# Kernel optimization log

Hardware: AMD Instinct MI355X
Metric: run time of the kernel (lower is better)

## Reference

```python
import jax, jax.numpy as jnp
import numpy as np
import math

S, H, NH, HD = 2048, 1280, 16, 80
WIN = 64
NW = S // WIN
I = 3420
OUT = 3584
L = 8
FULL_IDX = (3, 7)
MERGE = 4  # spatial_merge_size**2
EPS = 1e-6


def setup_inputs() -> dict:
    key = jax.random.key(0)
    ks = jax.random.split(key, 16)
    w = lambda k, s: jax.random.normal(k, s, jnp.float32) * 0.02
    # rotary tables: half-dim freqs duplicated, as in Qwen2.5-VL vision rotary
    inv_freq = 1.0 / (10000.0 ** (np.arange(0, HD // 2, dtype=np.float32) / (HD // 2)))
    freqs = np.outer(np.arange(S, dtype=np.float32), inv_freq)  # [S, HD/2]
    emb = np.concatenate([freqs, freqs], axis=-1)               # [S, HD]
    return {
        "hidden_states": jax.random.normal(ks[0], (S, H), jnp.float32),
        "full_attn_masks": jnp.ones((1, 1, S, S), jnp.float32),
        "window_attn_masks": jnp.ones((NW, 1, WIN, WIN), jnp.float32),
        "cos": jnp.asarray(np.cos(emb)),
        "sin": jnp.asarray(np.sin(emb)),
        "qkv_w": w(ks[1], (L, 3 * H, H)),
        "qkv_b": w(ks[2], (L, 3 * H)),
        "proj_w": w(ks[3], (L, H, H)),
        "proj_b": w(ks[4], (L, H)),
        "norm1_w": jnp.ones((L, H), jnp.float32),
        "norm2_w": jnp.ones((L, H), jnp.float32),
        "gate_w": w(ks[5], (L, I, H)),
        "gate_b": w(ks[6], (L, I)),
        "up_w": w(ks[7], (L, I, H)),
        "up_b": w(ks[8], (L, I)),
        "down_w": w(ks[9], (L, H, I)),
        "down_b": w(ks[10], (L, H)),
        "ln_q_w": jnp.ones((H,), jnp.float32),
        "m0_w": w(ks[11], (H * MERGE, H * MERGE)),
        "m0_b": w(ks[12], (H * MERGE,)),
        "m2_w": w(ks[13], (OUT, H * MERGE)),
        "m2_b": w(ks[14], (OUT,)),
    }


def rmsnorm(x, w):
    v = jnp.mean(jnp.square(x.astype(jnp.float32)), axis=-1, keepdims=True)
    return (x * jax.lax.rsqrt(v + EPS)) * w


def rotate_half(x):
    x1, x2 = jnp.split(x, 2, axis=-1)
    return jnp.concatenate([-x2, x1], axis=-1)


def apply_rope(q, k, cos, sin):
    return q * cos + rotate_half(q) * sin, k * cos + rotate_half(k) * sin


def attn_full(x, mask, cos, sin, qkv_w, qkv_b, proj_w, proj_b):
    # x: [S, H]; mask: [1, 1, S, S] (additive)
    qkv = (x @ qkv_w.T + qkv_b).reshape(S, 3, NH, HD)
    q, k, v = [t[:, i].transpose(1, 0, 2) for i, t in [(0, qkv), (1, qkv), (2, qkv)]]  # [NH, S, HD]
    q, k = apply_rope(q, k, cos, sin)  # cos/sin [S, HD] broadcast over heads
    aw = jnp.einsum('hsd,htd->hst', q, k) / math.sqrt(HD) + mask[0]
    aw = jax.nn.softmax(aw.astype(jnp.float32), axis=-1)
    o = jnp.einsum('hst,htd->hsd', aw, v).transpose(1, 0, 2).reshape(S, NH * HD)
    return o @ proj_w.T + proj_b


def attn_window(x, mask, cos, sin, qkv_w, qkv_b, proj_w, proj_b):
    xw = x.reshape(NW, WIN, H)
    qkv = (xw @ qkv_w.T + qkv_b).reshape(NW, WIN, 3, NH, HD).transpose(2, 0, 3, 1, 4)
    q, k, v = qkv[0], qkv[1], qkv[2]
    cw = cos.reshape(NW, 1, WIN, HD)
    sw = sin.reshape(NW, 1, WIN, HD)
    q, k = apply_rope(q, k, cw, sw)
    aw = jnp.einsum('whsd,whtd->whst', q, k) / math.sqrt(HD) + mask
    aw = jax.nn.softmax(aw.astype(jnp.float32), axis=-1)
    o = jnp.einsum('whst,whtd->whsd', aw, v).transpose(0, 2, 1, 3).reshape(S, NH * HD)
    return o @ proj_w.T + proj_b


def reference(hidden_states, full_attn_masks, window_attn_masks, cos, sin,
              qkv_w, qkv_b, proj_w, proj_b, norm1_w, norm2_w,
              gate_w, gate_b, up_w, up_b, down_w, down_b,
              ln_q_w, m0_w, m0_b, m2_w, m2_b):
    NEG = jnp.finfo(jnp.float32).min
    fm = (1.0 - full_attn_masks) * NEG
    wm = (1.0 - window_attn_masks) * NEG
    x = hidden_states
    for i in range(L):
        h = rmsnorm(x, norm1_w[i])
        if i in FULL_IDX:
            a = attn_full(h, fm, cos, sin, qkv_w[i], qkv_b[i], proj_w[i], proj_b[i])
        else:
            a = attn_window(h, wm, cos, sin, qkv_w[i], qkv_b[i], proj_w[i], proj_b[i])
        x = x + a
        h = rmsnorm(x, norm2_w[i])
        mlp = (jax.nn.silu(h @ gate_w[i].T + gate_b[i]) * (h @ up_w[i].T + up_b[i])) @ down_w[i].T + down_b[i]
        x = x + mlp
    # patch merger: RMSNorm -> merge 4 tokens -> Linear-GELU-Linear
    h = rmsnorm(x, ln_q_w).reshape(-1, H * MERGE)  # [S/4, 5120]
    h = jax.nn.gelu(h @ m0_w.T + m0_b, approximate=False)
    return h @ m2_w.T + m2_b  # [S/4, OUT]
```

## Files before the change

kernel.cpp:

```cpp
#include <hip/hip_runtime.h>
#include <hip/hip_bf16.h>
#include <math.h>

#define S_LEN 2048
#define HID   1280
#define NHEADS 16
#define HDIM  80
#define HDP   96
#define VROWS 96
#define LAYERS 8
#define IDIM  3420
#define IDIMP 3456
#define MERGED 5120
#define OUTD  3584
#define NCH   8
#define CHLEN 256
#define LWE   19824640LL

typedef __attribute__((ext_vector_type(8))) short short8;
typedef __attribute__((ext_vector_type(4))) float f32x4;
typedef __attribute__((ext_vector_type(16))) float f32x16;
typedef unsigned int u32;
typedef __attribute__((ext_vector_type(4))) u32 u32x4;
typedef __attribute__((address_space(1))) const u32* gptr_t;
typedef __attribute__((address_space(3))) u32* lptr_t;

__device__ inline unsigned short f2b(float f){
  __hip_bfloat16 b = __float2bfloat16(f);
  return __builtin_bit_cast(unsigned short, b);
}
__device__ inline float b2f(unsigned short u){
  return __bfloat162float(__builtin_bit_cast(__hip_bfloat16, u));
}
__device__ inline unsigned pk2(float lo, float hi){
  return (unsigned)f2b(lo) | ((unsigned)f2b(hi) << 16);
}

#define NSEG 42
struct ConvSegs {
  int bpre[NSEG + 1];
  long long srcoff[NSEG];
  long long dstoff[NSEG];
  int srcbase[NSEG];
  int N[NSEG], K[NSEG], Kp[NSEG];
  int rstride[NSEG], roffs[NSEG];
};

__global__ __launch_bounds__(256) void convert_all_kernel(
    ConvSegs cs,
    const float* __restrict__ b0, const float* __restrict__ b1,
    const float* __restrict__ b2, const float* __restrict__ b3,
    const float* __restrict__ b4, const float* __restrict__ b5,
    const float* __restrict__ b6,
    unsigned short* __restrict__ dst)
{
  const int b = blockIdx.x;
  int seg = 0;
  while (seg < NSEG - 1 && cs.bpre[seg + 1] <= b) ++seg;
  const int Kp = cs.Kp[seg], K = cs.K[seg], N = cs.N[seg];
  const int kg = Kp >> 3;
  size_t g = (size_t)(b - cs.bpre[seg]) * 256 + threadIdx.x;
  int k8 = (int)(g % kg);
  int n  = (int)(g / kg);
  int k0 = k8 * 8;
  const float* base;
  switch (cs.srcbase[seg]){
    case 0: base = b0; break; case 1: base = b1; break;
    case 2: base = b2; break; case 3: base = b3; break;
    case 4: base = b4; break; case 5: base = b5; break;
    default: base = b6; break;
  }
  const float* src = base + cs.srcoff[seg];
  u32 out0, out1, out2, out3;
  if (n < N && k0 + 8 <= K){
    const float* s = src + (size_t)n * K + k0;
    f32x4 f0 = __builtin_nontemporal_load((const f32x4*)s);
    f32x4 f1 = __builtin_nontemporal_load((const f32x4*)(s + 4));
    out0 = pk2(f0[0], f0[1]); out1 = pk2(f0[2], f0[3]);
    out2 = pk2(f1[0], f1[1]); out3 = pk2(f1[2], f1[3]);
  } else {
    u32 tmp[4];
    #pragma unroll
    for (int j = 0; j < 4; ++j){
      int ka = k0 + 2 * j;
      float lv = (n < N && ka     < K) ? src[(size_t)n * K + ka]     : 0.f;
      float hv = (n < N && ka + 1 < K) ? src[(size_t)n * K + ka + 1] : 0.f;
      tmp[j] = pk2(lv, hv);
    }
    out0 = tmp[0]; out1 = tmp[1]; out2 = tmp[2]; out3 = tmp[3];
  }
  size_t de = (size_t)cs.dstoff[seg] +
              ((size_t)n * cs.rstride[seg] + cs.roffs[seg]) * Kp + k0;
  u32x4 ov = {out0, out1, out2, out3};
  __builtin_nontemporal_store(ov, (u32x4*)(dst + de));
}

__global__ __launch_bounds__(256) void concat_bias_kernel(
    const float* __restrict__ g, const float* __restrict__ u, float* __restrict__ o)
{
  int L = blockIdx.y;
  int n = blockIdx.x * 256 + threadIdx.x;
  if (n >= 2 * IDIMP) return;
  int c = n >> 1, which = n & 1;
  float v = 0.f;
  if (c < IDIM) v = which ? u[(size_t)L * IDIM + c] : g[(size_t)L * IDIM + c];
  o[(size_t)L * 2 * IDIMP + n] = v;
}

__global__ __launch_bounds__(256) void rmsnorm_kernel(
    const float* __restrict__ x, const float* __restrict__ w,
    unsigned short* __restrict__ out, int H)
{
  int s = blockIdx.x;
  const float* row = x + (size_t)s * H;
  float ss = 0.f;
  for (int c = threadIdx.x; c < H; c += 256){ float v = row[c]; ss += v * v; }
  #pragma unroll
  for (int off = 32; off >= 1; off >>= 1) ss += __shfl_xor(ss, off, 64);
  __shared__ float red[4];
  if ((threadIdx.x & 63) == 0) red[threadIdx.x >> 6] = ss;
  __syncthreads();
  ss = red[0] + red[1] + red[2] + red[3];
  float rs = rsqrtf(ss / H + 1e-6f);
  unsigned short* orow = out + (size_t)s * H;
  for (int c = threadIdx.x; c < H; c += 256) orow[c] = f2b(row[c] * rs * w[c]);
}

template<int EPI, int BM>
__global__ __launch_bounds__(256) void gemm_kernel(
    const unsigned short* __restrict__ A, int lda,
    const unsigned short* __restrict__ B, int ldb,
    const float* __restrict__ bias, int Nact,
    void* __restrict__ Cv, int ldc,
    const float* __restrict__ res,
    int K)
{
  constexpr int MI = BM / 32;
  __shared__ __align__(16) unsigned short As[2][BM * 32];
  __shared__ __align__(16) unsigned short Bs[2][4096];
  const int tid  = threadIdx.x;
  const int lane = tid & 63;
  const int wave = tid >> 6;
  const int wm = wave >> 1, wn = wave & 1;
  const int m0 = blockIdx.y * BM, n0 = blockIdx.x * 128;
  const int l16 = lane & 15, lh = lane >> 4;
  const int lrow = lane >> 2;
  const int lcol = lane & 3;
  f32x4 acc[MI][4] = {};

  auto stage = [&](int bufi, int k0){
    #pragma unroll
    for (int j = 0; j < BM / 64; ++j){
      int chunk = wave * (BM / 64) + j;
      int row  = chunk * 16 + lrow;
      int slot = lcol ^ ((row >> 1) & 3);
      const unsigned short* srcA = A + (size_t)(m0 + row) * lda + k0 + slot * 8;
      __builtin_amdgcn_global_load_lds((gptr_t)srcA, (lptr_t)&As[bufi][chunk * 512], 16, 0, 0);
    }
    #pragma unroll
    for (int j = 0; j < 2; ++j){
      int chunk = wave * 2 + j;
      int row  = chunk * 16 + lrow;
      int slot = lcol ^ ((row >> 1) & 3);
      const unsigned short* srcB = B + (size_t)(n0 + row) * ldb + k0 + slot * 8;
      __builtin_amdgcn_global_load_lds((gptr_t)srcB, (lptr_t)&Bs[bufi][chunk * 512], 16, 0, 0);
    }
  };

  const int nt = K >> 5;
  stage(0, 0);
  __syncthreads();
  int buf = 0;
  for (int t = 0; t < nt; ++t){
    if (t + 1 < nt) stage(buf ^ 1, (t + 1) << 5);
    short8 af[MI], bfr[4];
    #pragma unroll
    for (int mi = 0; mi < MI; ++mi){
      int r = wm * (BM / 2) + mi * 16 + l16;
      int sl = lh ^ ((r >> 1) & 3);
      af[mi] = *(const short8*)&As[buf][r * 32 + sl * 8];
    }
    #pragma unroll
    for (int ni = 0; ni < 4; ++ni){
      int r = wn * 64 + ni * 16 + l16;
      int sl = lh ^ ((r >> 1) & 3);
      bfr[ni] = *(const short8*)&Bs[buf][r * 32 + sl * 8];
    }
    #pragma unroll
    for (int mi = 0; mi < MI; ++mi)
      #pragma unroll
      for (int ni = 0; ni < 4; ++ni)
        acc[mi][ni] = __builtin_amdgcn_mfma_f32_16x16x32_bf16(af[mi], bfr[ni], acc[mi][ni], 0, 0, 0);
    __syncthreads();
    buf ^= 1;
  }

  #pragma unroll
  for (int mi = 0; mi < MI; ++mi){
    int row = m0 + wm * (BM / 2) + mi * 16 + lh * 4;
    #pragma unroll
    for (int ni = 0; ni < 4; ++ni){
      int gn = n0 + wn * 64 + ni * 16 + l16;
      float bv = (gn < Nact) ? bias[gn] : 0.f;
      #pragma unroll
      for (int r2 = 0; r2 < 4; ++r2){
        float v = acc[mi][ni][r2] + bv;
        if (EPI == 4){
          float partner = __shfl_xor(v, 1);
          if (!(l16 & 1)){
            float r = v / (1.f + __expf(-v)) * partner;
            ((unsigned short*)Cv)[(size_t)(row + r2) * ldc + (gn >> 1)] = f2b(r);
          }
        } else {
          size_t offc = (size_t)(row + r2) * ldc + gn;
          if (EPI == 0)      ((float*)Cv)[offc] = v;
          else if (EPI == 1) ((float*)Cv)[offc] = res[offc] + v;
          else if (EPI == 2) ((unsigned short*)Cv)[offc] = f2b(0.5f * v * (1.0f + erff(v * 0.70710678118f)));
          else               ((unsigned short*)Cv)[offc] = f2b(v);
        }
      }
    }
  }
}

__global__ __launch_bounds__(256) void rope_split_kernel(
    const unsigned short* __restrict__ qkv, const float* __restrict__ cosT,
    const float* __restrict__ sinT,
    unsigned short* __restrict__ qo, unsigned short* __restrict__ ko,
    unsigned short* __restrict__ vt)
{
  __shared__ unsigned short vtile[80][128];
  const int h = blockIdx.x;
  const int s0 = blockIdx.y * 128;
  const int t = threadIdx.x;
  const int sr = t >> 1, half = t & 1;
  const int s = s0 + sr;
  const unsigned short* row = qkv + (size_t)s * 3840 + h * 80;
  const float* crow = cosT + (size_t)s * 80;
  const float* srow = sinT + (size_t)s * 80;
  const float sgn = half ? 1.f : -1.f;
  #pragma unroll
  for (int g = 0; g < 5; ++g){
    int d  = half * 40 + g * 8;
    int dp = 40 - half * 40 + g * 8;
    short8 q8  = *(const short8*)(row + d);
    short8 k8  = *(const short8*)(row + 1280 + d);
    short8 qp8 = *(const short8*)(row + dp);
    short8 kp8 = *(const short8*)(row + 1280 + dp);
    short8 v8  = *(const short8*)(row + 2560 + d);
    f32x4 c0  = *(const f32x4*)(crow + d);
    f32x4 c1  = *(const f32x4*)(crow + d + 4);
    f32x4 sn0 = *(const f32x4*)(srow + d);
    f32x4 sn1 = *(const f32x4*)(srow + d + 4);
    float cc[8] = {c0[0], c0[1], c0[2], c0[3], c1[0], c1[1], c1[2], c1[3]};
    float ss[8] = {sn0[0], sn0[1], sn0[2], sn0[3], sn1[0], sn1[1], sn1[2], sn1[3]};
    short8 qo8, ko8;
    #pragma unroll
    for (int j = 0; j < 8; ++j){
      float qv = b2f((unsigned short)q8[j]);
      float kv = b2f((unsigned short)k8[j]);
      float qr = sgn * b2f((unsigned short)qp8[j]);
      float kr = sgn * b2f((unsigned short)kp8[j]);
      qo8[j] = (short)f2b(qv * cc[j] + qr * ss[j]);
      ko8[j] = (short)f2b(kv * cc[j] + kr * ss[j]);
      vtile[d + j][sr] = (unsigned short)v8[j];
    }
    size_t qkoff = ((size_t)h * S_LEN + s) * HDP + d;
    *(short8*)(qo + qkoff) = qo8;
    *(short8*)(ko + qkoff) = ko8;
  }
  {
    short8 z = {};
    size_t poff = ((size_t)h * S_LEN + s) * HDP + 80 + half * 8;
    *(short8*)(qo + poff) = z;
    *(short8*)(ko + poff) = z;
  }
  __syncthreads();
  #pragma unroll
  for (int it = 0; it < 5; ++it){
    int j = t + it * 256;
    int d = j >> 4, ch = j & 15;
    u32x4 v = *(const u32x4*)&vtile[d][ch * 8];
    *(u32x4*)(vt + ((size_t)h * VROWS + d) * S_LEN + s0 + ch * 8) = v;
  }
}

template<int PART>
__global__ __launch_bounds__(256) void flash_kernel(
    const unsigned short* __restrict__ q, const unsigned short* __restrict__ k,
    const unsigned short* __restrict__ vt, unsigned short* __restrict__ out,
    float* __restrict__ opart, float* __restrict__ mlpart)
{
  __shared__ unsigned short ot[4][32][88];
  const int lane = threadIdx.x & 63;
  const int w = threadIdx.x >> 6;
  const int h = blockIdx.y;
  const int l31 = lane & 31, lh1 = lane >> 5;
  const int qr = blockIdx.x * 128 + w * 32;
  const int ch = PART ? blockIdx.z : 0;
  const unsigned short* qh = q + (size_t)h * S_LEN * HDP;
  const unsigned short* kh = k + (size_t)h * S_LEN * HDP;
  const unsigned short* vh = vt + (size_t)h * VROWS * S_LEN;

  short8 qa[5];
  #pragma unroll
  for (int kc = 0; kc < 5; ++kc)
    qa[kc] = *(const short8*)(qh + (size_t)(qr + l31) * HDP + kc * 16 + lh1 * 8);

  float m_ = -1e30f, l_ = 0.f;
  f32x16 o0 = {}, o1 = {}, o2 = {};
  const int kvb = PART ? ch * CHLEN : (qr & ~63);
  const int kve = PART ? ch * CHLEN + CHLEN : (qr & ~63) + 64;
  const float scale = 0.11180339887498949f;

  for (int kvt = kvb; kvt < kve; kvt += 32){
    f32x16 sc = {};
    __builtin_amdgcn_s_setprio(1);
    #pragma unroll
    for (int kc = 0; kc < 5; ++kc){
      short8 kf = *(const short8*)(kh + (size_t)(kvt + l31) * HDP + kc * 16 + lh1 * 8);
      sc = __builtin_amdgcn_mfma_f32_32x32x16_bf16(kf, qa[kc], sc, 0, 0, 0);
    }
    __builtin_amdgcn_s_setprio(0);
    float t = sc[0];
    #pragma unroll
    for (int i = 1; i < 16; ++i) t = fmaxf(t, sc[i]);
    t = fmaxf(t, __shfl_xor(t, 32)) * scale;
    if (!__all(t <= m_ + 8.f)){
      float mnew = fmaxf(m_, t);
      float corr = __expf(m_ - mnew);
      l_ *= corr;
      #pragma unroll
      for (int i = 0; i < 16; ++i){ o0[i] *= corr; o1[i] *= corr; o2[i] *= corr; }
      m_ = mnew;
    }
    float p[16];
    float rs = 0.f;
    #pragma unroll
    for (int i = 0; i < 16; ++i){ p[i] = __expf(sc[i] * scale - m_); rs += p[i]; }
    rs += __shfl_xor(rs, 32);
    l_ += rs;
    unsigned wd0[4], wd1[4];
    #pragma unroll
    for (int j = 0; j < 2; ++j){
      unsigned Aj = pk2(p[2 * j],     p[2 * j + 1]);
      unsigned Bj = pk2(p[4 + 2 * j], p[4 + 2 * j + 1]);
      unsigned t0 = __shfl_xor(Aj, 32);
      unsigned t1 = __shfl_xor(Bj, 32);
      wd0[j]     = lh1 ? t1 : Aj;
      wd0[2 + j] = lh1 ? Bj : t0;
      Aj = pk2(p[8 + 2 * j],  p[8 + 2 * j + 1]);
      Bj = pk2(p[12 + 2 * j], p[12 + 2 * j + 1]);
      t0 = __shfl_xor(Aj, 32);
      t1 = __shfl_xor(Bj, 32);
      wd1[j]     = lh1 ? t1 : Aj;
      wd1[2 + j] = lh1 ? Bj : t0;
    }
    __builtin_amdgcn_s_setprio(1);
    #pragma unroll
    for (int kc2 = 0; kc2 < 2; ++kc2){
      u32x4 uw = kc2 ? u32x4{wd1[0], wd1[1], wd1[2], wd1[3]}
                     : u32x4{wd0[0], wd0[1], wd0[2], wd0[3]};
      short8 pb = __builtin_bit_cast(short8, uw);
      const unsigned short* vb = vh + kvt + kc2 * 16 + lh1 * 8;
      o0 = __builtin_amdgcn_mfma_f32_32x32x16_bf16(
          *(const short8*)(vb + (size_t)(l31)      * S_LEN), pb, o0, 0, 0, 0);
      o1 = __builtin_amdgcn_mfma_f32_32x32x16_bf16(
          *(const short8*)(vb + (size_t)(32 + l31) * S_LEN), pb, o1, 0, 0, 0);
      o2 = __builtin_amdgcn_mfma_f32_32x32x16_bf16(
          *(const short8*)(vb + (size_t)(64 + l31) * S_LEN), pb, o2, 0, 0, 0);
    }
    __builtin_amdgcn_s_setprio(0);
  }

  if (PART){
    const size_t hb = (size_t)(ch * NHEADS + h) * 80;
    #pragma unroll
    for (int r = 0; r < 16; ++r){
      int dl = (r & 3) + 8 * (r >> 2) + 4 * lh1;
      opart[(hb + dl)      * S_LEN + qr + l31] = o0[r];
      opart[(hb + 32 + dl) * S_LEN + qr + l31] = o1[r];
      if (dl < 16) opart[(hb + 64 + dl) * S_LEN + qr + l31] = o2[r];
    }
    if (lane < 32){
      size_t mb = ((size_t)(ch * NHEADS + h) * S_LEN + qr + l31) * 2;
      mlpart[mb] = m_; mlpart[mb + 1] = l_;
    }
  } else {
    float inv = 1.f / l_;
    #pragma unroll
    for (int r = 0; r < 16; ++r){
      int dl = (r & 3) + 8 * (r >> 2) + 4 * lh1;
      ot[w][l31][dl]      = f2b(o0[r] * inv);
      ot[w][l31][32 + dl] = f2b(o1[r] * inv);
      if (dl < 16) ot[w][l31][64 + dl] = f2b(o2[r] * inv);
    }
    int qq = lane >> 1, half = lane & 1;
    #pragma unroll
    for (int j = 0; j < 20; ++j){
      unsigned v = *(const unsigned*)&ot[w][qq][half * 40 + j * 2];
      *(unsigned*)&out[(size_t)(qr + qq) * HID + h * HDIM + half * 40 + j * 2] = v;
    }
  }
}

__global__ __launch_bounds__(256) void flash_reduce_kernel(
    const float* __restrict__ opart, const float* __restrict__ mlpart,
    unsigned short* __restrict__ out)
{
  __shared__ float wn[NCH][256];
  __shared__ unsigned short ot[256][82];
  const int tid = threadIdx.x;
  const int h = blockIdx.y;
  const int q0 = blockIdx.x * 256;
  float mv[NCH], lv[NCH];
  float M = -1e30f;
  #pragma unroll
  for (int c = 0; c < NCH; ++c){
    size_t mb = ((size_t)(c * NHEADS + h) * S_LEN + q0 + tid) * 2;
    mv[c] = mlpart[mb]; lv[c] = mlpart[mb + 1];
    M = fmaxf(M, mv[c]);
  }
  float L = 0.f;
  #pragma unroll
  for (int c = 0; c < NCH; ++c){ mv[c] = __expf(mv[c] - M); L += mv[c] * lv[c]; }
  float invL = 1.f / L;
  #pragma unroll
  for (int c = 0; c < NCH; ++c) wn[c][tid] = mv[c] * invL;
  __syncthreads();
  for (int d = 0; d < HDIM; ++d){
    float acc = 0.f;
    #pragma unroll
    for (int c = 0; c < NCH; ++c)
      acc += wn[c][tid] * opart[((size_t)(c * NHEADS + h) * 80 + d) * S_LEN + q0 + tid];
    ot[tid][d] = f2b(acc);
  }
  __syncthreads();
  #pragma unroll
  for (int j = 0; j < 40; ++j){
    unsigned v = *(const unsigned*)&ot[tid][j * 2];
    *(unsigned*)&out[(size_t)(q0 + tid) * HID + h * HDIM + j * 2] = v;
  }
}

extern "C" void kernel_launch(void* const* d_in, const int* in_sizes, int n_in,
                              void* d_out, int out_size, void* d_ws, size_t ws_size,
                              hipStream_t stream)
{
  const float* hidden = (const float*)d_in[0];
  const float* cosT   = (const float*)d_in[3];
  const float* sinT   = (const float*)d_in[4];
  const float* qkv_w  = (const float*)d_in[5];
  const float* qkv_b  = (const float*)d_in[6];
  const float* proj_w = (const float*)d_in[7];
  const float* proj_b = (const float*)d_in[8];
  const float* norm1_w= (const float*)d_in[9];
  const float* norm2_w= (const float*)d_in[10];
  const float* gate_w = (const float*)d_in[11];
  const float* gate_b = (const float*)d_in[12];
  const float* up_w   = (const float*)d_in[13];
  const float* up_b   = (const float*)d_in[14];
  const float* down_w = (const float*)d_in[15];
  const float* down_b = (const float*)d_in[16];
  const float* ln_q_w = (const float*)d_in[17];
  const float* m0_w   = (const float*)d_in[18];
  const float* m0_b   = (const float*)d_in[19];
  const float* m2_w   = (const float*)d_in[20];
  const float* m2_b   = (const float*)d_in[21];

  char* ws = (char*)d_ws;
  size_t off = 0;
  auto carve = [&](size_t bytes)->char*{
    char* p = ws + off; off += (bytes + 255) & ~(size_t)255; return p;
  };
  float*          x    = (float*)         carve((size_t)S_LEN * HID * 4);
  unsigned short* hbuf = (unsigned short*)carve((size_t)S_LEN * HID * 2);
  unsigned short* qkvb = (unsigned short*)carve((size_t)S_LEN * 3840 * 2);
  unsigned short* qp   = (unsigned short*)carve((size_t)NHEADS * S_LEN * HDP * 2);
  unsigned short* kp   = (unsigned short*)carve((size_t)NHEADS * S_LEN * HDP * 2);
  unsigned short* vtb  = (unsigned short*)carve((size_t)NHEADS * VROWS * S_LEN * 2);
  unsigned short* ao   = (unsigned short*)carve((size_t)S_LEN * HID * 2);
  unsigned short* mlp  = (unsigned short*)carve((size_t)S_LEN * IDIMP * 2);
  unsigned short* mg   = (unsigned short*)carve((size_t)512 * MERGED * 2);
  float*          opart= (float*)         carve((size_t)NCH * NHEADS * 80 * S_LEN * 4);
  float*          mlpt = (float*)         carve((size_t)NCH * NHEADS * S_LEN * 2 * 4);
  float*          cbias= (float*)         carve((size_t)LAYERS * 2 * IDIMP * 4);
  unsigned short* wbf  = (unsigned short*)carve((size_t)203161600 * 2);
  (void)ws_size; (void)in_sizes; (void)n_in; (void)out_size;

  ConvSegs cs;
  int totalblocks = 0;
  {
    int si = 0;
    auto add = [&](int base, long long soff, long long doff, int N, int K,
                   int Np, int Kp, int rstride, int roffs){
      cs.bpre[si] = totalblocks;
      cs.srcbase[si] = base; cs.srcoff[si] = soff; cs.dstoff[si] = doff;
      cs.N[si] = N; cs.K[si] = K; cs.Kp[si] = Kp;
      cs.rstride[si] = rstride; cs.roffs[si] = roffs;
      long long groups = (long long)Np * (Kp >> 3);
      totalblocks += (int)((groups + 255) / 256);
      ++si;
    };
    for (long long i = 0; i < LAYERS; ++i){
      add(0, i * 3840LL * HID,        i * LWE + 0,        3840, HID, 3840, HID, 1, 0);
      add(1, i * (long long)HID * HID, i * LWE + 4915200,  HID, HID, HID, HID, 1, 0);
      add(2, i * (long long)IDIM * HID, i * LWE + 6553600,  IDIM, HID, IDIMP, HID, 2, 0);
      add(3, i * (long long)IDIM * HID, i * LWE + 6553600,  IDIM, HID, IDIMP, HID, 2, 1);
      add(4, i * (long long)HID * IDIM, i * LWE + 15400960, HID, IDIM, HID, IDIMP, 1, 0);
    }
    add(5, 0, 8 * LWE,            MERGED, MERGED, MERGED, MERGED, 1, 0);
    add(6, 0, 8 * LWE + 26214400, OUTD,   MERGED, OUTD,   MERGED, 1, 0);
    cs.bpre[NSEG] = totalblocks;
  }

  convert_all_kernel<<<totalblocks, 256, 0, stream>>>(
      cs, qkv_w, proj_w, gate_w, up_w, down_w, m0_w, m2_w, wbf);
  concat_bias_kernel<<<dim3(27, LAYERS), 256, 0, stream>>>(gate_b, up_b, cbias);
  hipMemcpyAsync(x, hidden, (size_t)S_LEN * HID * 4, hipMemcpyDeviceToDevice, stream);

  for (int i = 0; i < LAYERS; ++i){
    unsigned short* wl = wbf + (size_t)i * LWE;
    unsigned short* wqkv = wl;
    unsigned short* wproj= wl + 4915200;
    unsigned short* wgu  = wl + 6553600;
    unsigned short* wdown= wl + 15400960;

    rmsnorm_kernel<<<S_LEN, 256, 0, stream>>>(x, norm1_w + (size_t)i * HID, hbuf, HID);
    gemm_kernel<3,128><<<dim3(30, 16), 256, 0, stream>>>(
        hbuf, HID, wqkv, HID, qkv_b + (size_t)i * 3840, 3840,
        qkvb, 3840, nullptr, HID);
    rope_split_kernel<<<dim3(NHEADS, 16), 256, 0, stream>>>(qkvb, cosT, sinT, qp, kp, vtb);
    if (i == 3 || i == 7){
      flash_kernel<1><<<dim3(16, 16, NCH), 256, 0, stream>>>(qp, kp, vtb, nullptr, opart, mlpt);
      flash_reduce_kernel<<<dim3(8, 16), 256, 0, stream>>>(opart, mlpt, ao);
    } else {
      flash_kernel<0><<<dim3(16, 16), 256, 0, stream>>>(qp, kp, vtb, ao, nullptr, nullptr);
    }
    gemm_kernel<1,64><<<dim3(10, 32), 256, 0, stream>>>(
        ao, HID, wproj, HID, proj_b + (size_t)i * HID, HID,
        x, HID, x, HID);
    rmsnorm_kernel<<<S_LEN, 256, 0, stream>>>(x, norm2_w + (size_t)i * HID, hbuf, HID);
    gemm_kernel<4,128><<<dim3(54, 16), 256, 0, stream>>>(
        hbuf, HID, wgu, HID, cbias + (size_t)i * 2 * IDIMP, 2 * IDIMP,
        mlp, IDIMP, nullptr, HID);
    gemm_kernel<1,64><<<dim3(10, 32), 256, 0, stream>>>(
        mlp, IDIMP, wdown, IDIMP, down_b + (size_t)i * HID, HID,
        x, HID, x, IDIMP);
  }
  unsigned short* wm0 = wbf + 8 * LWE;
  unsigned short* wm2 = wm0 + (size_t)MERGED * MERGED;
  rmsnorm_kernel<<<S_LEN, 256, 0, stream>>>(x, ln_q_w, hbuf, HID);
  gemm_kernel<2,64><<<dim3(40, 8), 256, 0, stream>>>(
      hbuf, MERGED, wm0, MERGED, m0_b, MERGED, mg, MERGED, nullptr, MERGED);
  gemm_kernel<0,64><<<dim3(28, 8), 256, 0, stream>>>(
      mg, MERGED, wm2, MERGED, m2_b, OUTD, d_out, OUTD, nullptr, MERGED);
}
```

Measured before the change: 2.593 ms.

## Fuse full-attention split-KV reduction into flash kernel and remap blocks across XCDs

Full-attention layers now split the KV range across the four waves of one block (32 queries per block, 512 keys per wave). The partial results are combined in shared memory, which removes the separate reduce kernel and the fp32 partial-output round trip through global memory. Separately, the GEMM, rope and flash kernels remap block IDs so that neighbouring tiles land on the same XCD, aiming for better L2 locality. The in-block reduction adds several __syncthreads and serialized accumulation rounds. It also gives fewer, longer-running blocks for full attention.

Result: no change. 2.582 ms (-0.4%).

```diff
diff --git a/kernel.cpp b/kernel.cpp
--- a/kernel.cpp
+++ b/kernel.cpp
@@ -13,8 +13,6 @@
 #define IDIMP 3456
 #define MERGED 5120
 #define OUTD  3584
-#define NCH   8
-#define CHLEN 256
 #define LWE   19824640LL
 
 typedef __attribute__((ext_vector_type(8))) short short8;
@@ -142,7 +140,13 @@
   const int lane = tid & 63;
   const int wave = tid >> 6;
   const int wm = wave >> 1, wn = wave & 1;
-  const int m0 = blockIdx.y * BM, n0 = blockIdx.x * 128;
+  const int gx = gridDim.x, gy = gridDim.y;
+  const int total = gx * gy;
+  const int orig = blockIdx.y * gx + blockIdx.x;
+  const int q8 = total >> 3, r8 = total & 7;
+  const int xcd = orig & 7, loc = orig >> 3;
+  const int wg = (xcd < r8 ? xcd * (q8 + 1) : r8 * (q8 + 1) + (xcd - r8) * q8) + loc;
+  const int m0 = (wg % gy) * BM, n0 = (wg / gy) * 128;
   const int l16 = lane & 15, lh = lane >> 4;
   const int lrow = lane >> 2;
   const int lcol = lane & 3;
@@ -230,8 +234,10 @@
     unsigned short* __restrict__ vt)
 {
   __shared__ unsigned short vtile[80][128];
-  const int h = blockIdx.x;
-  const int s0 = blockIdx.y * 128;
+  int id = blockIdx.y * 16 + blockIdx.x;
+  int logical = ((id & 7) << 5) + (id >> 3);
+  const int h = logical & 15;
+  const int s0 = (logical >> 4) * 128;
   const int t = threadIdx.x;
   const int sr = t >> 1, half = t & 1;
   const int s = s0 + sr;
@@ -288,16 +294,21 @@
 template<int PART>
 __global__ __launch_bounds__(256) void flash_kernel(
     const unsigned short* __restrict__ q, const unsigned short* __restrict__ k,
-    const unsigned short* __restrict__ vt, unsigned short* __restrict__ out,
-    float* __restrict__ opart, float* __restrict__ mlpart)
-{
-  __shared__ unsigned short ot[4][32][88];
+    const unsigned short* __restrict__ vt, unsigned short* __restrict__ out)
+{
   const int lane = threadIdx.x & 63;
   const int w = threadIdx.x >> 6;
-  const int h = blockIdx.y;
   const int l31 = lane & 31, lh1 = lane >> 5;
-  const int qr = blockIdx.x * 128 + w * 32;
-  const int ch = PART ? blockIdx.z : 0;
+  int h, qr;
+  if (PART){
+    int id = blockIdx.y * gridDim.x + blockIdx.x;
+    int logical = ((id & 7) << 7) + (id >> 3);
+    h = logical >> 6; qr = (logical & 63) * 32;
+  } else {
+    int id = blockIdx.y * gridDim.x + blockIdx.x;
+    int logical = ((id & 7) << 5) + (id >> 3);
+    h = logical >> 4; qr = (logical & 15) * 128 + w * 32;
+  }
   const unsigned short* qh = q + (size_t)h * S_LEN * HDP;
   const unsigned short* kh = k + (size_t)h * S_LEN * HDP;
   const unsigned short* vh = vt + (size_t)h * VROWS * S_LEN;
@@ -309,8 +320,8 @@
 
   float m_ = -1e30f, l_ = 0.f;
   f32x16 o0 = {}, o1 = {}, o2 = {};
-  const int kvb = PART ? ch * CHLEN : (qr & ~63);
-  const int kve = PART ? ch * CHLEN + CHLEN : (qr & ~63) + 64;
+  const int kvb = PART ? w * 512 : (qr & ~63);
+  const int kve = PART ? w * 512 + 512 : (qr & ~63) + 64;
   const float scale = 0.11180339887498949f;
 
   for (int kvt = kvb; kvt < kve; kvt += 32){
@@ -374,19 +385,54 @@
   }
 
   if (PART){
-    const size_t hb = (size_t)(ch * NHEADS + h) * 80;
-    #pragma unroll
-    for (int r = 0; r < 16; ++r){
-      int dl = (r & 3) + 8 * (r >> 2) + 4 * lh1;
-      opart[(hb + dl)      * S_LEN + qr + l31] = o0[r];
-      opart[(hb + 32 + dl) * S_LEN + qr + l31] = o1[r];
-      if (dl < 16) opart[(hb + 64 + dl) * S_LEN + qr + l31] = o2[r];
-    }
-    if (lane < 32){
-      size_t mb = ((size_t)(ch * NHEADS + h) * S_LEN + qr + l31) * 2;
-      mlpart[mb] = m_; mlpart[mb + 1] = l_;
+    __shared__ float of[80][33];
+    __shared__ float mlsh[4][32][2];
+    __shared__ float Lsh[32];
+    __shared__ unsigned short ot2[32][88];
+    if (lane < 32){ mlsh[w][l31][0] = m_; mlsh[w][l31][1] = l_; }
+    __syncthreads();
+    float M = fmaxf(fmaxf(mlsh[0][l31][0], mlsh[1][l31][0]),
+                    fmaxf(mlsh[2][l31][0], mlsh[3][l31][0]));
+    float L = 0.f;
+    #pragma unroll
+    for (int c = 0; c < 4; ++c) L += __expf(mlsh[c][l31][0] - M) * mlsh[c][l31][1];
+    float wgt = __expf(m_ - M);
+    if (w == 0 && lane < 32) Lsh[l31] = L;
+    #pragma unroll
+    for (int rnd = 0; rnd < 4; ++rnd){
+      if (w == rnd){
+        #pragma unroll
+        for (int i = 0; i < 16; ++i){
+          int dl = (i & 3) + 8 * (i >> 2) + 4 * lh1;
+          if (rnd == 0){
+            of[dl][l31]      = wgt * o0[i];
+            of[32 + dl][l31] = wgt * o1[i];
+            if (dl < 16) of[64 + dl][l31] = wgt * o2[i];
+          } else {
+            of[dl][l31]      += wgt * o0[i];
+            of[32 + dl][l31] += wgt * o1[i];
+            if (dl < 16) of[64 + dl][l31] += wgt * o2[i];
+          }
+        }
+      }
+      __syncthreads();
+    }
+    const int tq = threadIdx.x & 31, ds0 = (threadIdx.x >> 5) * 10;
+    float Lq = Lsh[tq];
+    #pragma unroll
+    for (int j = 0; j < 10; ++j)
+      ot2[tq][ds0 + j] = f2b(of[ds0 + j][tq] / Lq);
+    __syncthreads();
+    if (threadIdx.x < 64){
+      int qq = threadIdx.x >> 1, half = threadIdx.x & 1;
+      #pragma unroll
+      for (int j2 = 0; j2 < 20; ++j2){
+        unsigned v = *(const unsigned*)&ot2[qq][half * 40 + j2 * 2];
+        *(unsigned*)&out[(size_t)(qr + qq) * HID + h * HDIM + half * 40 + j2 * 2] = v;
+      }
     }
   } else {
+    __shared__ unsigned short ot[4][32][88];
     float inv = 1.f / l_;
     #pragma unroll
     for (int r = 0; r < 16; ++r){
@@ -401,45 +447,6 @@
       unsigned v = *(const unsigned*)&ot[w][qq][half * 40 + j * 2];
       *(unsigned*)&out[(size_t)(qr + qq) * HID + h * HDIM + half * 40 + j * 2] = v;
     }
-  }
-}
-
-__global__ __launch_bounds__(256) void flash_reduce_kernel(
-    const float* __restrict__ opart, const float* __restrict__ mlpart,
-    unsigned short* __restrict__ out)
-{
-  __shared__ float wn[NCH][256];
-  __shared__ unsigned short ot[256][82];
-  const int tid = threadIdx.x;
-  const int h = blockIdx.y;
-  const int q0 = blockIdx.x * 256;
-  float mv[NCH], lv[NCH];
-  float M = -1e30f;
-  #pragma unroll
-  for (int c = 0; c < NCH; ++c){
-    size_t mb = ((size_t)(c * NHEADS + h) * S_LEN + q0 + tid) * 2;
-    mv[c] = mlpart[mb]; lv[c] = mlpart[mb + 1];
-    M = fmaxf(M, mv[c]);
-  }
-  float L = 0.f;
-  #pragma unroll
-  for (int c = 0; c < NCH; ++c){ mv[c] = __expf(mv[c] - M); L += mv[c] * lv[c]; }
-  float invL = 1.f / L;
-  #pragma unroll
-  for (int c = 0; c < NCH; ++c) wn[c][tid] = mv[c] * invL;
-  __syncthreads();
-  for (int d = 0; d < HDIM; ++d){
-    float acc = 0.f;
-    #pragma unroll
-    for (int c = 0; c < NCH; ++c)
-      acc += wn[c][tid] * opart[((size_t)(c * NHEADS + h) * 80 + d) * S_LEN + q0 + tid];
-    ot[tid][d] = f2b(acc);
-  }
-  __syncthreads();
-  #pragma unroll
-  for (int j = 0; j < 40; ++j){
-    unsigned v = *(const unsigned*)&ot[tid][j * 2];
-    *(unsigned*)&out[(size_t)(q0 + tid) * HID + h * HDIM + j * 2] = v;
   }
 }
 
@@ -482,8 +489,6 @@
   unsigned short* ao   = (unsigned short*)carve((size_t)S_LEN * HID * 2);
   unsigned short* mlp  = (unsigned short*)carve((size_t)S_LEN * IDIMP * 2);
   unsigned short* mg   = (unsigned short*)carve((size_t)512 * MERGED * 2);
-  float*          opart= (float*)         carve((size_t)NCH * NHEADS * 80 * S_LEN * 4);
-  float*          mlpt = (float*)         carve((size_t)NCH * NHEADS * S_LEN * 2 * 4);
   float*          cbias= (float*)         carve((size_t)LAYERS * 2 * IDIMP * 4);
   unsigned short* wbf  = (unsigned short*)carve((size_t)203161600 * 2);
   (void)ws_size; (void)in_sizes; (void)n_in; (void)out_size;
@@ -532,10 +537,9 @@
         qkvb, 3840, nullptr, HID);
     rope_split_kernel<<<dim3(NHEADS, 16), 256, 0, stream>>>(qkvb, cosT, sinT, qp, kp, vtb);
     if (i == 3 || i == 7){
-      flash_kernel<1><<<dim3(16, 16, NCH), 256, 0, stream>>>(qp, kp, vtb, nullptr, opart, mlpt);
-      flash_reduce_kernel<<<dim3(8, 16), 256, 0, stream>>>(opart, mlpt, ao);
+      flash_kernel<1><<<dim3(64, 16), 256, 0, stream>>>(qp, kp, vtb, ao);
     } else {
-      flash_kernel<0><<<dim3(16, 16), 256, 0, stream>>>(qp, kp, vtb, ao, nullptr, nullptr);
+      flash_kernel<0><<<dim3(16, 16), 256, 0, stream>>>(qp, kp, vtb, ao);
     }
     gemm_kernel<1,64><<<dim3(10, 32), 256, 0, stream>>>(
         ao, HID, wproj, HID, proj_b + (size_t)i * HID, HID,
```
